# Kernel optimization log

Measured on AMD Instinct MI355X. Metric: run time of the kernel, lower is better.

The kernel has to match this reference:

```python
import jax, jax.numpy as jnp
import numpy as np

N = 43
H = N // 2  # 21


def _mk(key, i, o):
    kw, kb = jax.random.split(key)
    bound = 1.0 / np.sqrt(i)
    W = jax.random.uniform(kw, (i, o), jnp.float32, -bound, bound)
    b = jax.random.uniform(kb, (o,), jnp.float32, -bound, bound)
    return W, b


def setup_inputs() -> dict:
    key = jax.random.key(0)
    keys = jax.random.split(key, 11)
    x = jax.random.normal(keys[0], (1048576, N), jnp.float32)
    dims = [(N, N), (N, N), (N, N), (N, N), (N, H),  # encoder
            (H, N), (N, N), (N, N), (N, N), (N, N)]  # decoder
    out = {"x": x}
    for li, (i, o) in enumerate(dims):
        W, b = _mk(keys[li + 1], i, o)
        out[f"W{li}"] = W
        out[f"b{li}"] = b
    return out


def reference(x, W0, b0, W1, b1, W2, b2, W3, b3, W4, b4,
              W5, b5, W6, b6, W7, b7, W8, b8, W9, b9):
    Ws = [W0, W1, W2, W3, W4, W5, W6, W7, W8, W9]
    bs = [b0, b1, b2, b3, b4, b5, b6, b7, b8, b9]
    h = x
    for li in range(10):
        h = h @ Ws[li] + bs[li]
        # tanh after every layer except encoder bottleneck (4) and final (9)
        if li not in (4, 9):
            h = jnp.tanh(h)
    return h
```

## Files before the change

kernel.cpp:

```cpp
#include <hip/hip_runtime.h>


typedef __fp16 pk16x2 __attribute__((ext_vector_type(2)));
typedef _Float16 f16x8 __attribute__((ext_vector_type(8)));
typedef float f32x4 __attribute__((ext_vector_type(4)));
typedef unsigned u32x4 __attribute__((ext_vector_type(4)));

#define TPB 1024
#define NBLK 256
#define ITERS 8
#define NROWS 1048576
#define NCOL 43
#define ROWB 172u
#define XBYTES ((size_t)NROWS * ROWB)
#define WSTRIDE 72
#define SLOT_ROWS 44
#define WSLOT (SLOT_ROWS * WSTRIDE)
#define W_BYTES (10 * WSLOT * 2)
#define XBUF_BYTES 6144
#define X_BASE W_BYTES
#define SMEM_BYTES (X_BASE + 16 * XBUF_BYTES)

__device__ __forceinline__ float fast_tanh(float x) {
  float t = __builtin_amdgcn_exp2f(x * 2.8853900817779268f);
  float r = __builtin_amdgcn_rcpf(t + 1.0f);
  return __builtin_fmaf(-2.0f, r, 1.0f);
}

__device__ __forceinline__ unsigned pk2(float a, float b) {
  pk16x2 h = __builtin_amdgcn_cvt_pkrtz(a, b);
  return __builtin_bit_cast(unsigned, h);
}

__device__ __forceinline__ void issue_dma(const char* xc, const char* xlim,
                                          char* xb, unsigned rowbytes,
                                          int lane) {
  const char* base = xc + rowbytes;
#pragma unroll
  for (int c = 0; c < 6; ++c) {
    const char* src = base + c * 1024 + lane * 16;
    src = (src > xlim) ? xlim : src;
    __builtin_amdgcn_global_load_lds(
        (const __attribute__((address_space(1))) void*)src,
        (__attribute__((address_space(3))) void*)(xb + c * 1024), 16, 0, 0);
  }
}

struct FragsV { f16x8 s0c0, s0c1, s1c0, s1c1; };

template <int NT, int KC, bool DOTANH, int NLOUT, int KCN>
__device__ __forceinline__ FragsV layer_fwd(const _Float16* __restrict__ Wl,
                                            FragsV Bi, int g, int lr) {
  f16x8 Bv[2][2];
  Bv[0][0] = Bi.s0c0; Bv[0][1] = Bi.s0c1;
  Bv[1][0] = Bi.s1c0; Bv[1][1] = Bi.s1c1;

  f32x4 acc[3][2];
#pragma unroll
  for (int t = 0; t < NT; ++t)
#pragma unroll
    for (int s = 0; s < 2; ++s) acc[t][s] = f32x4{0.f, 0.f, 0.f, 0.f};

#pragma unroll
  for (int c = 0; c < KC; ++c)
#pragma unroll
    for (int t = 0; t < NT; ++t) {
      f16x8 A = *(const f16x8*)(Wl + (16 * t + lr) * WSTRIDE + 8 * g + 32 * c);
#pragma unroll
      for (int s = 0; s < 2; ++s)
        acc[t][s] = __builtin_amdgcn_mfma_f32_16x16x32_f16(A, Bv[s][c],
                                                           acc[t][s], 0, 0, 0);
    }

  f16x8 oc0[2], oc1[2];
#pragma unroll
  for (int s = 0; s < 2; ++s) {
    unsigned pk[3][2];
#pragma unroll
    for (int t = 0; t < NT; ++t) {
      float v[4];
#pragma unroll
      for (int r = 0; r < 4; ++r) {
        float u = acc[t][s][r];
        if (DOTANH) u = fast_tanh(u);
        if (t == (NLOUT >> 4)) {
          int col = 16 * t + 4 * g + r;
          u = (col == NLOUT) ? 1.0f : u;
        }
        v[r] = u;
      }
      pk[t][0] = pk2(v[0], v[1]);
      pk[t][1] = pk2(v[2], v[3]);
    }
    u32x4 d0 = {pk[0][0], pk[0][1], pk[1][0], pk[1][1]};
    oc0[s] = __builtin_bit_cast(f16x8, d0);
    if (KCN == 2) {
      u32x4 d1 = {pk[NT - 1][0], pk[NT - 1][1], 0u, 0u};
      oc1[s] = __builtin_bit_cast(f16x8, d1);
    } else {
      oc1[s] = oc0[s];
    }
  }
  FragsV O;
  O.s0c0 = oc0[0]; O.s0c1 = oc1[0];
  O.s1c0 = oc0[1]; O.s1c1 = oc1[1];
  return O;
}

extern "C" __global__ void __launch_bounds__(TPB)
ae_kernel(const float* __restrict__ x,
          const float* __restrict__ W0, const float* __restrict__ B0,
          const float* __restrict__ W1, const float* __restrict__ B1,
          const float* __restrict__ W2, const float* __restrict__ B2,
          const float* __restrict__ W3, const float* __restrict__ B3,
          const float* __restrict__ W4, const float* __restrict__ B4,
          const float* __restrict__ W5, const float* __restrict__ B5,
          const float* __restrict__ W6, const float* __restrict__ B6,
          const float* __restrict__ W7, const float* __restrict__ B7,
          const float* __restrict__ W8, const float* __restrict__ B8,
          const float* __restrict__ W9, const float* __restrict__ B9,
          float* __restrict__ out) {
  extern __shared__ char smem[];
  _Float16* lw = (_Float16*)smem;

  const int tid = threadIdx.x;
  const int wave = tid >> 6;
  const int lane = tid & 63;
  const int g = lane >> 4;
  const int lr = lane & 15;

  {
    const float* Wp[10] = {W0, W1, W2, W3, W4, W5, W6, W7, W8, W9};
    const float* Bp[10] = {B0, B1, B2, B3, B4, B5, B6, B7, B8, B9};
    const int KLs[10] = {43, 43, 43, 43, 43, 21, 43, 43, 43, 43};
    const int NLs[10] = {43, 43, 43, 43, 21, 43, 43, 43, 43, 43};
#pragma unroll
    for (int L = 0; L < 10; ++L) {
      const float* Wl = Wp[L];
      const float* Bl = Bp[L];
      const int KL = KLs[L], NL = NLs[L];
      for (int idx = tid; idx < SLOT_ROWS * 64; idx += TPB) {
        int n = idx >> 6, kp = idx & 63;
        float v = 0.0f;
        if (n < NL) {
          int c = kp >> 5, g2 = (kp >> 3) & 3, j = kp & 7;
          int F;
          if (L == 0) F = kp;
          else if (c == 0) F = 16 * (j >> 2) + 4 * g2 + (j & 3);
          else if (j < 4)  F = 32 + 4 * g2 + j;
          else             F = 63;
          if (F < KL) v = Wl[F * NL + n];
          else if (F == KL) v = Bl[n];
        }
        lw[L * WSLOT + n * WSTRIDE + kp] = (_Float16)v;
      }
    }
  }

  __syncthreads();

  const char* xc = (const char*)x;
  const char* xlim = xc + (XBYTES - 16);
  const unsigned blockbase = (unsigned)blockIdx.x * (ITERS * 512) + wave * 32;
  float* xb = (float*)(smem + X_BASE + wave * XBUF_BYTES);

  issue_dma(xc, xlim, (char*)xb, blockbase * ROWB, lane);

#pragma unroll 1
  for (int it = 0; it < ITERS; ++it) {
    const unsigned row0 = blockbase + (unsigned)it * 512u;

    asm volatile("s_waitcnt vmcnt(0)" ::: "memory");

    FragsV B;
#pragma unroll
    for (int s = 0; s < 2; ++s) {
      const float* xr = xb + (16 * s + lr) * NCOL;
      float f0[8], f1[8];
#pragma unroll
      for (int j = 0; j < 8; ++j) {
        f0[j] = xr[8 * g + j];
        f1[j] = xr[32 + 8 * g + j];
      }
      float e3 = (g == 1) ? 1.0f : f1[3];
      u32x4 d0 = {pk2(f0[0], f0[1]), pk2(f0[2], f0[3]),
                  pk2(f0[4], f0[5]), pk2(f0[6], f0[7])};
      u32x4 d1 = {pk2(f1[0], f1[1]), pk2(f1[2], e3),
                  pk2(f1[4], f1[5]), pk2(f1[6], f1[7])};
      if (s == 0) { B.s0c0 = __builtin_bit_cast(f16x8, d0);
                    B.s0c1 = __builtin_bit_cast(f16x8, d1); }
      else        { B.s1c0 = __builtin_bit_cast(f16x8, d0);
                    B.s1c1 = __builtin_bit_cast(f16x8, d1); }
    }

    asm volatile("s_waitcnt lgkmcnt(0)" ::: "memory");
    if (it + 1 < ITERS)
      issue_dma(xc, xlim, (char*)xb, (row0 + 512u) * ROWB, lane);

    B = layer_fwd<3, 2, true, 43, 2>(lw + 0 * WSLOT, B, g, lr);
    B = layer_fwd<3, 2, true, 43, 2>(lw + 1 * WSLOT, B, g, lr);
    B = layer_fwd<3, 2, true, 43, 2>(lw + 2 * WSLOT, B, g, lr);
    B = layer_fwd<3, 2, true, 43, 2>(lw + 3 * WSLOT, B, g, lr);
    B = layer_fwd<2, 2, false, 21, 1>(lw + 4 * WSLOT, B, g, lr);
    B = layer_fwd<3, 1, true, 43, 2>(lw + 5 * WSLOT, B, g, lr);
    B = layer_fwd<3, 2, true, 43, 2>(lw + 6 * WSLOT, B, g, lr);
    B = layer_fwd<3, 2, true, 43, 2>(lw + 7 * WSLOT, B, g, lr);
    B = layer_fwd<3, 2, true, 43, 2>(lw + 8 * WSLOT, B, g, lr);

    {
      f16x8 Bv[2][2];
      Bv[0][0] = B.s0c0; Bv[0][1] = B.s0c1;
      Bv[1][0] = B.s1c0; Bv[1][1] = B.s1c1;
      f32x4 a9[3][2];
#pragma unroll
      for (int t = 0; t < 3; ++t)
#pragma unroll
        for (int s = 0; s < 2; ++s) a9[t][s] = f32x4{0.f, 0.f, 0.f, 0.f};
#pragma unroll
      for (int c = 0; c < 2; ++c)
#pragma unroll
        for (int t = 0; t < 3; ++t) {
          f16x8 A = *(const f16x8*)(lw + 9 * WSLOT + (16 * t + lr) * WSTRIDE +
                                    8 * g + 32 * c);
#pragma unroll
          for (int s = 0; s < 2; ++s)
            a9[t][s] = __builtin_amdgcn_mfma_f32_16x16x32_f16(A, Bv[s][c],
                                                              a9[t][s], 0, 0, 0);
        }
#pragma unroll
      for (int t = 0; t < 3; ++t)
#pragma unroll
        for (int s = 0; s < 2; ++s)
#pragma unroll
          for (int r = 0; r < 4; ++r) {
            int col = 16 * t + 4 * g + r;
            if (col < NCOL)
              out[(size_t)(row0 + 16 * s + lr) * NCOL + col] = a9[t][s][r];
          }
    }
  }
}

extern "C" void kernel_launch(void* const* d_in, const int* in_sizes, int n_in,
                              void* d_out, int out_size, void* d_ws,
                              size_t ws_size, hipStream_t stream) {
  const float* x = (const float*)d_in[0];
  const float* W[10];
  const float* B[10];
  for (int i = 0; i < 10; ++i) {
    W[i] = (const float*)d_in[1 + 2 * i];
    B[i] = (const float*)d_in[2 + 2 * i];
  }
  (void)hipFuncSetAttribute(reinterpret_cast<const void*>(ae_kernel),
                            hipFuncAttributeMaxDynamicSharedMemorySize,
                            SMEM_BYTES);
  ae_kernel<<<dim3(NBLK), dim3(TPB), SMEM_BYTES, stream>>>(
      x, W[0], B[0], W[1], B[1], W[2], B[2], W[3], B[3], W[4], B[4],
      W[5], B[5], W[6], B[6], W[7], B[7], W[8], B[8], W[9], B[9],
      (float*)d_out);
}
```

Before: 137.3 us.

## Pad staged input rows in LDS for vector reads and simplify MFMA init/stores

The global-to-LDS DMA now scatters each 172-byte input row into a 192-byte padded slot, so each lane can fetch its fragment with 16-byte LDS vector loads instead of many scalar float reads. The first MFMA of each layer uses a shared zero accumulator operand instead of explicitly zeroed registers. Output stores use precomputed byte offsets with a simpler column mask. The aim is to cut LDS read instructions and VALU overhead in the per-iteration prologue and epilogue. Per-lane DMA offsets are held in registers, which adds some register pressure.

After: 137.5 us. No clear change (+0.2%).

```diff
diff --git a/kernel.cpp b/kernel.cpp
--- a/kernel.cpp
+++ b/kernel.cpp
@@ -19,7 +19,7 @@
 #define W_BYTES (10 * WSLOT * 2)
 #define XBUF_BYTES 6144
 #define X_BASE W_BYTES
-#define SMEM_BYTES (X_BASE + 16 * XBUF_BYTES)
+#define SMEM_BYTES (X_BASE + 16 * XBUF_BYTES + 64)
 
 __device__ __forceinline__ float fast_tanh(float x) {
   float t = __builtin_amdgcn_exp2f(x * 2.8853900817779268f);
@@ -32,37 +32,26 @@
   return __builtin_bit_cast(unsigned, h);
 }
 
-__device__ __forceinline__ void issue_dma(const char* xc, const char* xlim,
-                                          char* xb, unsigned rowbytes,
-                                          int lane) {
-  const char* base = xc + rowbytes;
-#pragma unroll
-  for (int c = 0; c < 6; ++c) {
-    const char* src = base + c * 1024 + lane * 16;
-    src = (src > xlim) ? xlim : src;
-    __builtin_amdgcn_global_load_lds(
-        (const __attribute__((address_space(1))) void*)src,
-        (__attribute__((address_space(3))) void*)(xb + c * 1024), 16, 0, 0);
-  }
-}
-
 struct FragsV { f16x8 s0c0, s0c1, s1c0, s1c1; };
 
 template <int NT, int KC, bool DOTANH, int NLOUT, int KCN>
 __device__ __forceinline__ FragsV layer_fwd(const _Float16* __restrict__ Wl,
-                                            FragsV Bi, int g, int lr) {
+                                            FragsV Bi, f32x4 Z, int g, int lr) {
   f16x8 Bv[2][2];
   Bv[0][0] = Bi.s0c0; Bv[0][1] = Bi.s0c1;
   Bv[1][0] = Bi.s1c0; Bv[1][1] = Bi.s1c1;
 
   f32x4 acc[3][2];
 #pragma unroll
-  for (int t = 0; t < NT; ++t)
-#pragma unroll
-    for (int s = 0; s < 2; ++s) acc[t][s] = f32x4{0.f, 0.f, 0.f, 0.f};
-
-#pragma unroll
-  for (int c = 0; c < KC; ++c)
+  for (int t = 0; t < NT; ++t) {
+    f16x8 A = *(const f16x8*)(Wl + (16 * t + lr) * WSTRIDE + 8 * g);
+#pragma unroll
+    for (int s = 0; s < 2; ++s)
+      acc[t][s] = __builtin_amdgcn_mfma_f32_16x16x32_f16(A, Bv[s][0], Z,
+                                                         0, 0, 0);
+  }
+#pragma unroll
+  for (int c = 1; c < KC; ++c)
 #pragma unroll
     for (int t = 0; t < NT; ++t) {
       f16x8 A = *(const f16x8*)(Wl + (16 * t + lr) * WSTRIDE + 8 * g + 32 * c);
@@ -157,14 +146,33 @@
     }
   }
 
+  unsigned dmaoff[6];
+#pragma unroll
+  for (int i = 0; i < 6; ++i) {
+    unsigned u = 64u * i + (unsigned)lane;
+    dmaoff[i] = (u / 12u) * ROWB + (u % 12u) * 16u;
+  }
+
   __syncthreads();
 
   const char* xc = (const char*)x;
   const char* xlim = xc + (XBYTES - 16);
   const unsigned blockbase = (unsigned)blockIdx.x * (ITERS * 512) + wave * 32;
   float* xb = (float*)(smem + X_BASE + wave * XBUF_BYTES);
-
-  issue_dma(xc, xlim, (char*)xb, blockbase * ROWB, lane);
+  const f32x4 Z = {0.f, 0.f, 0.f, 0.f};
+
+  {
+    const char* base = xc + blockbase * ROWB;
+#pragma unroll
+    for (int i = 0; i < 6; ++i) {
+      const char* src = base + dmaoff[i];
+      src = (src > xlim) ? xlim : src;
+      __builtin_amdgcn_global_load_lds(
+          (const __attribute__((address_space(1))) void*)src,
+          (__attribute__((address_space(3))) void*)((char*)xb + i * 1024),
+          16, 0, 0);
+    }
+  }
 
 #pragma unroll 1
   for (int it = 0; it < ITERS; ++it) {
@@ -175,18 +183,16 @@
     FragsV B;
 #pragma unroll
     for (int s = 0; s < 2; ++s) {
-      const float* xr = xb + (16 * s + lr) * NCOL;
-      float f0[8], f1[8];
-#pragma unroll
-      for (int j = 0; j < 8; ++j) {
-        f0[j] = xr[8 * g + j];
-        f1[j] = xr[32 + 8 * g + j];
-      }
-      float e3 = (g == 1) ? 1.0f : f1[3];
-      u32x4 d0 = {pk2(f0[0], f0[1]), pk2(f0[2], f0[3]),
-                  pk2(f0[4], f0[5]), pk2(f0[6], f0[7])};
-      u32x4 d1 = {pk2(f1[0], f1[1]), pk2(f1[2], e3),
-                  pk2(f1[4], f1[5]), pk2(f1[6], f1[7])};
+      const float* xr = xb + (16 * s + lr) * 48;
+      f32x4 q0 = *(const f32x4*)(xr + 8 * g);
+      f32x4 q1 = *(const f32x4*)(xr + 8 * g + 4);
+      f32x4 q2 = *(const f32x4*)(xr + 32 + 8 * g);
+      f32x4 q3 = *(const f32x4*)(xr + 36 + 8 * g);
+      float e3 = (g == 1) ? 1.0f : q2[3];
+      u32x4 d0 = {pk2(q0[0], q0[1]), pk2(q0[2], q0[3]),
+                  pk2(q1[0], q1[1]), pk2(q1[2], q1[3])};
+      u32x4 d1 = {pk2(q2[0], q2[1]), pk2(q2[2], e3),
+                  pk2(q3[0], q3[1]), pk2(q3[2], q3[3])};
       if (s == 0) { B.s0c0 = __builtin_bit_cast(f16x8, d0);
                     B.s0c1 = __builtin_bit_cast(f16x8, d1); }
       else        { B.s1c0 = __builtin_bit_cast(f16x8, d0);
@@ -194,18 +200,28 @@
     }
 
     asm volatile("s_waitcnt lgkmcnt(0)" ::: "memory");
-    if (it + 1 < ITERS)
-      issue_dma(xc, xlim, (char*)xb, (row0 + 512u) * ROWB, lane);
-
-    B = layer_fwd<3, 2, true, 43, 2>(lw + 0 * WSLOT, B, g, lr);
-    B = layer_fwd<3, 2, true, 43, 2>(lw + 1 * WSLOT, B, g, lr);
-    B = layer_fwd<3, 2, true, 43, 2>(lw + 2 * WSLOT, B, g, lr);
-    B = layer_fwd<3, 2, true, 43, 2>(lw + 3 * WSLOT, B, g, lr);
-    B = layer_fwd<2, 2, false, 21, 1>(lw + 4 * WSLOT, B, g, lr);
-    B = layer_fwd<3, 1, true, 43, 2>(lw + 5 * WSLOT, B, g, lr);
-    B = layer_fwd<3, 2, true, 43, 2>(lw + 6 * WSLOT, B, g, lr);
-    B = layer_fwd<3, 2, true, 43, 2>(lw + 7 * WSLOT, B, g, lr);
-    B = layer_fwd<3, 2, true, 43, 2>(lw + 8 * WSLOT, B, g, lr);
+    if (it + 1 < ITERS) {
+      const char* base = xc + (row0 + 512u) * ROWB;
+#pragma unroll
+      for (int i = 0; i < 6; ++i) {
+        const char* src = base + dmaoff[i];
+        src = (src > xlim) ? xlim : src;
+        __builtin_amdgcn_global_load_lds(
+            (const __attribute__((address_space(1))) void*)src,
+            (__attribute__((address_space(3))) void*)((char*)xb + i * 1024),
+            16, 0, 0);
+      }
+    }
+
+    B = layer_fwd<3, 2, true, 43, 2>(lw + 0 * WSLOT, B, Z, g, lr);
+    B = layer_fwd<3, 2, true, 43, 2>(lw + 1 * WSLOT, B, Z, g, lr);
+    B = layer_fwd<3, 2, true, 43, 2>(lw + 2 * WSLOT, B, Z, g, lr);
+    B = layer_fwd<3, 2, true, 43, 2>(lw + 3 * WSLOT, B, Z, g, lr);
+    B = layer_fwd<2, 2, false, 21, 1>(lw + 4 * WSLOT, B, Z, g, lr);
+    B = layer_fwd<3, 1, true, 43, 2>(lw + 5 * WSLOT, B, Z, g, lr);
+    B = layer_fwd<3, 2, true, 43, 2>(lw + 6 * WSLOT, B, Z, g, lr);
+    B = layer_fwd<3, 2, true, 43, 2>(lw + 7 * WSLOT, B, Z, g, lr);
+    B = layer_fwd<3, 2, true, 43, 2>(lw + 8 * WSLOT, B, Z, g, lr);
 
     {
       f16x8 Bv[2][2];
@@ -213,29 +229,32 @@
       Bv[1][0] = B.s1c0; Bv[1][1] = B.s1c1;
       f32x4 a9[3][2];
 #pragma unroll
+      for (int t = 0; t < 3; ++t) {
+        f16x8 A = *(const f16x8*)(lw + 9 * WSLOT + (16 * t + lr) * WSTRIDE +
+                                  8 * g);
+#pragma unroll
+        for (int s = 0; s < 2; ++s)
+          a9[t][s] = __builtin_amdgcn_mfma_f32_16x16x32_f16(A, Bv[s][0], Z,
+                                                            0, 0, 0);
+      }
+#pragma unroll
+      for (int t = 0; t < 3; ++t) {
+        f16x8 A = *(const f16x8*)(lw + 9 * WSLOT + (16 * t + lr) * WSTRIDE +
+                                  8 * g + 32);
+#pragma unroll
+        for (int s = 0; s < 2; ++s)
+          a9[t][s] = __builtin_amdgcn_mfma_f32_16x16x32_f16(A, Bv[s][1],
+                                                            a9[t][s], 0, 0, 0);
+      }
+      char* ob = (char*)out + ((size_t)(row0 + lr) * ROWB + 16u * g);
+#pragma unroll
       for (int t = 0; t < 3; ++t)
 #pragma unroll
-        for (int s = 0; s < 2; ++s) a9[t][s] = f32x4{0.f, 0.f, 0.f, 0.f};
-#pragma unroll
-      for (int c = 0; c < 2; ++c)
-#pragma unroll
-        for (int t = 0; t < 3; ++t) {
-          f16x8 A = *(const f16x8*)(lw + 9 * WSLOT + (16 * t + lr) * WSTRIDE +
-                                    8 * g + 32 * c);
-#pragma unroll
-          for (int s = 0; s < 2; ++s)
-            a9[t][s] = __builtin_amdgcn_mfma_f32_16x16x32_f16(A, Bv[s][c],
-                                                              a9[t][s], 0, 0, 0);
-        }
-#pragma unroll
-      for (int t = 0; t < 3; ++t)
-#pragma unroll
         for (int s = 0; s < 2; ++s)
 #pragma unroll
           for (int r = 0; r < 4; ++r) {
-            int col = 16 * t + 4 * g + r;
-            if (col < NCOL)
-              out[(size_t)(row0 + 16 * s + lr) * NCOL + col] = a9[t][s][r];
+            if (t < 2 || 4 * g + r < 11)
+              *(float*)(ob + 2752 * s + 64 * t + 4 * r) = a9[t][s][r];
           }
     }
   }
```
